# Kernel optimization log

Hardware: AMD Instinct MI355X
Metric: run time of the kernel (lower is better)

The kernel has to match this reference:

```python
import jax, jax.numpy as jnp
import numpy as np

B, S, D, H = 4, 2048, 512, 8
DEPTH = D // H
BAND = 16  # log_thresholds [1,2,4,8,16] union == distance <= 16


def setup_inputs() -> dict:
    key = jax.random.key(0)
    ks = jax.random.split(key, 11)
    sc = 0.02
    return {
        "q": jax.random.normal(ks[0], (B, S, D), jnp.float32),
        "k": jax.random.normal(ks[1], (B, S, D), jnp.float32),
        "v": jax.random.normal(ks[2], (B, S, D), jnp.float32),
        "wq": jax.random.normal(ks[3], (D, D), jnp.float32) * sc,
        "bq": jnp.zeros((D,), jnp.float32),
        "wk": jax.random.normal(ks[4], (D, D), jnp.float32) * sc,
        "bk": jnp.zeros((D,), jnp.float32),
        "wv": jax.random.normal(ks[5], (D, D), jnp.float32) * sc,
        "bv": jnp.zeros((D,), jnp.float32),
        "wo": jax.random.normal(ks[6], (D, D), jnp.float32) * sc,
        "bo": jnp.zeros((D,), jnp.float32),
    }


def _split_heads(x):
    # [B,S,D] -> [B,H,S,depth]
    b, s, _ = x.shape
    return x.reshape(b, s, H, DEPTH).transpose(0, 2, 1, 3)


def reference(q, k, v, wq, bq, wk, bk, wv, bv, wo, bo):
    qh = _split_heads(q @ wq + bq)
    kh = _split_heads(k @ wk + bk)
    vh = _split_heads(v @ wv + bv)
    scale = 1.0 / jnp.sqrt(jnp.float32(DEPTH))
    logits = jnp.einsum("bhqd,bhkd->bhqk", qh, kh) * scale  # [B,H,S,S]
    idx = jnp.arange(S)
    keep = jnp.abs(idx[:, None] - idx[None, :]) <= BAND  # band mask [S,S]
    logits = jnp.where(keep[None, None], logits, jnp.float32(-1e9))
    attn = jax.nn.softmax(logits, axis=-1)
    out = jnp.einsum("bhqk,bhkd->bhqd", attn, vh)
    out = out.transpose(0, 2, 1, 3).reshape(q.shape[0], -1, D)
    return out @ wo + bo
```

## Files before the change

### kernel.cpp

```cpp
#include <hip/hip_runtime.h>

typedef unsigned int uint;
typedef unsigned short ushort;
typedef __attribute__((ext_vector_type(8))) short bf16x8;
typedef __attribute__((ext_vector_type(4))) float f32x4;

namespace {
constexpr int kS = 2048;
constexpr int kD = 512;
constexpr int kH = 8;
constexpr int kBand = 16;

constexpr size_t kQpk = 0;
constexpr size_t kKpk = 4194304;
constexpr size_t kVpk = kKpk + 4259840;
constexpr size_t kObp = kVpk + 4259840;
constexpr size_t kApk = kObp + 4194304;
constexpr size_t kBpk = kApk + 12582912;
}

static __device__ __forceinline__ ushort f2bf(float f) {
  uint u = __builtin_bit_cast(uint, f);
  u = (u + 0x7fffu + ((u >> 16) & 1u)) >> 16;
  return (ushort)u;
}

static __device__ __forceinline__ bf16x8 cvt8(f32x4 lo, f32x4 hi) {
  uint4 r;
  asm("v_cvt_pk_bf16_f32 %0, %1, %2" : "=v"(r.x) : "v"(lo[0]), "v"(lo[1]));
  asm("v_cvt_pk_bf16_f32 %0, %1, %2" : "=v"(r.y) : "v"(lo[2]), "v"(lo[3]));
  asm("v_cvt_pk_bf16_f32 %0, %1, %2" : "=v"(r.z) : "v"(hi[0]), "v"(hi[1]));
  asm("v_cvt_pk_bf16_f32 %0, %1, %2" : "=v"(r.w) : "v"(hi[2]), "v"(hi[3]));
  return __builtin_bit_cast(bf16x8, r);
}

__global__ __launch_bounds__(256) void prep_all(
    const float* __restrict__ q, const float* __restrict__ k,
    const float* __restrict__ v, const float* __restrict__ wq,
    const float* __restrict__ wk, const float* __restrict__ wv,
    const float* __restrict__ wo, ushort* __restrict__ ws) {
  __shared__ float Ws[64][65];
  const int blk = blockIdx.x, tid = threadIdx.x;
  if (blk < 384) {
    const int z = blk >> 7, rb = blk & 127;
    const float* X = z == 0 ? q : (z == 1 ? k : v);
    ushort* A = ws + kApk + (size_t)z * 4194304 + (size_t)rb * 32768;
    const int tl = tid >> 2, dq = tid & 3;
    const float* src = X + (size_t)(rb * 64 + tl) * kD + dq * 8;
    ushort* dstb = A + (tl >> 4) * 512 + (dq * 16 + (tl & 15)) * 8;
#pragma unroll
    for (int c = 0; c < 16; ++c) {
      const f32x4 lo = *(const f32x4*)(src + c * 32);
      const f32x4 hi = *(const f32x4*)(src + c * 32 + 4);
      *(bf16x8*)(dstb + c * 2048) = cvt8(lo, hi);
    }
    return;
  }
  if (blk >= 640) {
    const int idx = blk - 640;
    const int bh = idx >> 1, gg = (idx & 1) * 64;
    ushort* p = ws + kVpk + ((size_t)(bh * 65 + gg) * 4) * 512 + tid * 8;
    *(uint4*)p = (uint4){0, 0, 0, 0};
    return;
  }
  const int w = blk - 384;
  const int z = w >> 6;
  const float* W = z == 0 ? wq : (z == 1 ? wk : (z == 2 ? wv : wo));
  const int kt = ((w >> 3) & 7) * 64, nt = (w & 7) * 64;
  const int r = tid >> 2, c0 = (tid & 3) * 16;
#pragma unroll
  for (int i = 0; i < 4; ++i) {
    const float4 x =
        *(const float4*)(W + (size_t)(kt + r) * kD + nt + c0 + i * 4);
    Ws[r][c0 + i * 4 + 0] = x.x;
    Ws[r][c0 + i * 4 + 1] = x.y;
    Ws[r][c0 + i * 4 + 2] = x.z;
    Ws[r][c0 + i * 4 + 3] = x.w;
  }
  __syncthreads();
  const int nl = tid >> 2, k0 = (tid & 3) * 16;
  alignas(16) ushort tmp[16];
#pragma unroll
  for (int i = 0; i < 16; ++i) tmp[i] = f2bf(Ws[k0 + i][nl]);
  const int ng = nt + nl, kg = kt + k0;
  const int c = ng >> 6, sub = (ng >> 4) & 3, l = ng & 15;
  const int it = kg >> 5, q0 = (kg >> 3) & 3;
  ushort* base = ws + kBpk + ((size_t)(z * 8 + c) * 16 + it) * 2048 +
                 (sub * 64 + l) * 8;
  *(uint4*)(base + q0 * 128) = *(const uint4*)&tmp[0];
  *(uint4*)(base + (q0 + 1) * 128) = *(const uint4*)&tmp[8];
}

__global__ __launch_bounds__(64) void gemm_qkv(
    const ushort* __restrict__ ws_c, ushort* __restrict__ ws,
    const float* __restrict__ bq, const float* __restrict__ bk,
    const float* __restrict__ bv) {
  __shared__ alignas(16) ushort Tl[64 * 72];

  const int lane = threadIdx.x, l15 = lane & 15, qd = lane >> 4;
  const int lin = blockIdx.x;
  const int xcd = lin & 7, j = lin >> 3;
  const int ct = j & 7;
  const int rtl = xcd + 8 * (j >> 3);
  const int mode = rtl >> 7, rt = rtl & 127;
  const int row0 = rt * 64;

  const float* bias = mode == 0 ? bq : (mode == 1 ? bk : bv);
  const ushort* pa =
      ws_c + kApk + (size_t)mode * 4194304 + (size_t)rt * 32768 + lane * 8;
  const ushort* pb =
      ws_c + kBpk + ((size_t)(mode * 8 + ct) * 16) * 2048 + lane * 8;

  f32x4 acc[4][4];
#pragma unroll
  for (int mi = 0; mi < 4; ++mi)
#pragma unroll
    for (int ni = 0; ni < 4; ++ni) acc[mi][ni] = (f32x4)(0.f);

  bf16x8 Af[3][4], Bf[3][4];
#define LDSET(s, itv)                                                  \
  {                                                                    \
    _Pragma("unroll") for (int x = 0; x < 4; ++x) {                    \
      Af[s][x] = *(const bf16x8*)(pa + (itv)*2048 + x * 512);          \
      Bf[s][x] = *(const bf16x8*)(pb + (itv)*2048 + x * 512);          \
    }                                                                  \
  }
  LDSET(0, 0);
  LDSET(1, 1);
#pragma unroll
  for (int it = 0; it < 16; ++it) {
    if (it < 14) LDSET((it + 2) % 3, it + 2);
    const int s = it % 3;
#pragma unroll
    for (int mi = 0; mi < 4; ++mi)
#pragma unroll
      for (int ni = 0; ni < 4; ++ni)
        acc[mi][ni] = __builtin_amdgcn_mfma_f32_16x16x32_bf16(
            Af[s][mi], Bf[s][ni], acc[mi][ni], 0, 0, 0);
  }
#undef LDSET

  float bcol[4];
#pragma unroll
  for (int ni = 0; ni < 4; ++ni) bcol[ni] = bias[ct * 64 + ni * 16 + l15];

  const int bh = (row0 >> 11) * kH + ct;
  if (mode <= 1) {
#pragma unroll
    for (int mi = 0; mi < 4; ++mi)
#pragma unroll
      for (int ni = 0; ni < 4; ++ni)
#pragma unroll
        for (int r = 0; r < 4; ++r)
          Tl[(mi * 16 + qd * 4 + r) * 72 + ni * 16 + l15] =
              f2bf(acc[mi][ni][r] + bcol[ni]);
    asm volatile("s_waitcnt lgkmcnt(0)" ::: "memory");
    const int s = (row0 & (kS - 1)) + lane;
    const int g = s >> 4;
    const ushort* Trow = &Tl[lane * 72];
    ushort* base =
        (mode == 0)
            ? ws + kQpk + ((size_t)(bh * 128 + g) * 2) * 512 + (s & 15) * 8
            : ws + kKpk + ((size_t)(bh * 130 + g + 1) * 2) * 512 + (s & 15) * 8;
#pragma unroll
    for (int cc = 0; cc < 8; ++cc)
      *(uint4*)(base + (cc >> 2) * 512 + (cc & 3) * 128) =
          *(const uint4*)&Trow[cc * 8];
  } else {
#pragma unroll
    for (int mi = 0; mi < 4; ++mi)
#pragma unroll
      for (int ni = 0; ni < 4; ++ni)
#pragma unroll
        for (int r = 0; r < 4; ++r)
          Tl[(ni * 16 + l15) * 72 + mi * 16 + qd * 4 + r] =
              f2bf(acc[mi][ni][r] + bcol[ni]);
    asm volatile("s_waitcnt lgkmcnt(0)" ::: "memory");
    const int nt = lane >> 4, l15v = lane & 15;
    const int sb = (row0 & (kS - 1)) + 16;
    const ushort* Trow = &Tl[lane * 72];
#pragma unroll
    for (int cc = 0; cc < 8; ++cc) {
      const int sc = sb + cc * 8;
      const int gg = sc >> 5, khc = (sc >> 3) & 3;
      ushort* dst = ws + kVpk + ((size_t)(bh * 65 + gg) * 4 + nt) * 512 +
                    khc * 128 + l15v * 8;
      *(uint4*)dst = *(const uint4*)&Trow[cc * 8];
    }
  }
}

__global__ __launch_bounds__(512) void attn_out(
    const ushort* __restrict__ ws_c, const float* __restrict__ bo,
    float* __restrict__ outp) {
  __shared__ alignas(16) ushort Pl[8 * 32 * 72];

  const int tid = threadIdx.x;
  const int w = tid >> 6, lane = tid & 63, l15 = lane & 15, qd = lane >> 4;
  const int b = blockIdx.y;
  const int q0 = blockIdx.x * 32;
  const int bh = b * kH + w;
  ushort* Plw = &Pl[w * 2304];

  const ushort* Qpk = ws_c + kQpk;
  const ushort* Kpk = ws_c + kKpk;
  const ushort* Vpk = ws_c + kVpk;

  bf16x8 qf[2][2], kf[4][2];
#pragma unroll
  for (int mi = 0; mi < 2; ++mi)
#pragma unroll
    for (int kc = 0; kc < 2; ++kc)
      qf[mi][kc] = *(const bf16x8*)&Qpk[((size_t)(bh * 128 + (q0 >> 4) + mi) *
                                            2 + kc) * 512 + lane * 8];
#pragma unroll
  for (int ni = 0; ni < 4; ++ni)
#pragma unroll
    for (int kc = 0; kc < 2; ++kc)
      kf[ni][kc] = *(const bf16x8*)&Kpk[((size_t)(bh * 130 + (q0 >> 4) + ni) *
                                            2 + kc) * 512 + lane * 8];

  f32x4 S[2][4];
#pragma unroll
  for (int mi = 0; mi < 2; ++mi)
#pragma unroll
    for (int ni = 0; ni < 4; ++ni) S[mi][ni] = (f32x4)(0.f);
#pragma unroll
  for (int mi = 0; mi < 2; ++mi)
#pragma unroll
    for (int ni = 0; ni < 4; ++ni)
#pragma unroll
      for (int kc = 0; kc < 2; ++kc)
        S[mi][ni] = __builtin_amdgcn_mfma_f32_16x16x32_bf16(
            qf[mi][kc], kf[ni][kc], S[mi][ni], 0, 0, 0);

#pragma unroll
  for (int mi = 0; mi < 2; ++mi)
#pragma unroll
    for (int ni = 0; ni < 4; ++ni)
#pragma unroll
      for (int r = 0; r < 4; ++r) {
        const int q_local = mi * 16 + qd * 4 + r;
        const int key_local = ni * 16 + l15;
        const int key = q0 - kBand + key_local;
        const int dlt = key_local - q_local;
        const bool ok = (dlt >= 0) && (dlt <= 32) && (key >= 0) && (key < kS);
        S[mi][ni][r] = ok ? S[mi][ni][r] * 0.125f : -3.0e38f;
      }

  float inv[2][4];
#pragma unroll
  for (int mi = 0; mi < 2; ++mi)
#pragma unroll
    for (int r = 0; r < 4; ++r) {
      float m = S[mi][0][r];
#pragma unroll
      for (int ni = 1; ni < 4; ++ni) m = fmaxf(m, S[mi][ni][r]);
      m = fmaxf(m, __shfl_xor(m, 1));
      m = fmaxf(m, __shfl_xor(m, 2));
      m = fmaxf(m, __shfl_xor(m, 4));
      m = fmaxf(m, __shfl_xor(m, 8));
      float s = 0.f;
#pragma unroll
      for (int ni = 0; ni < 4; ++ni) {
        const float e = __expf(S[mi][ni][r] - m);
        S[mi][ni][r] = e;
        s += e;
      }
      s += __shfl_xor(s, 1);
      s += __shfl_xor(s, 2);
      s += __shfl_xor(s, 4);
      s += __shfl_xor(s, 8);
      inv[mi][r] = 1.f / s;
    }

#pragma unroll
  for (int mi = 0; mi < 2; ++mi)
#pragma unroll
    for (int ni = 0; ni < 4; ++ni)
#pragma unroll
      for (int r = 0; r < 4; ++r)
        Plw[(mi * 16 + qd * 4 + r) * 72 + ni * 16 + l15] = f2bf(S[mi][ni][r]);
  asm volatile("s_waitcnt lgkmcnt(0)" ::: "memory");

  f32x4 O[2][4];
#pragma unroll
  for (int mi = 0; mi < 2; ++mi)
#pragma unroll
    for (int nt = 0; nt < 4; ++nt) O[mi][nt] = (f32x4)(0.f);

#pragma unroll
  for (int kc = 0; kc < 2; ++kc) {
    bf16x8 pf[2], vfr[4];
#pragma unroll
    for (int mi = 0; mi < 2; ++mi)
      pf[mi] = *(const bf16x8*)&Plw[(mi * 16 + l15) * 72 + kc * 32 + qd * 8];
#pragma unroll
    for (int nt = 0; nt < 4; ++nt)
      vfr[nt] = *(const bf16x8*)&Vpk[((size_t)(bh * 65 + (q0 >> 5) + kc) * 4 +
                                       nt) * 512 + lane * 8];
#pragma unroll
    for (int mi = 0; mi < 2; ++mi)
#pragma unroll
      for (int nt = 0; nt < 4; ++nt)
        O[mi][nt] = __builtin_amdgcn_mfma_f32_16x16x32_bf16(pf[mi], vfr[nt],
                                                            O[mi][nt], 0, 0, 0);
  }

#pragma unroll
  for (int mi = 0; mi < 2; ++mi)
#pragma unroll
    for (int nt = 0; nt < 4; ++nt)
#pragma unroll
      for (int r = 0; r < 4; ++r)
        Plw[(mi * 16 + qd * 4 + r) * 72 + nt * 16 + l15] =
            f2bf(O[mi][nt][r] * inv[mi][r]);

  __syncthreads();

  const ushort* pb =
      ws_c + kBpk + ((size_t)(3 * 8 + w) * 16) * 2048 + lane * 8;

  f32x4 acc[2][4];
#pragma unroll
  for (int mi = 0; mi < 2; ++mi)
#pragma unroll
    for (int ni = 0; ni < 4; ++ni) acc[mi][ni] = (f32x4)(0.f);

  bf16x8 Bf[2][4];
#pragma unroll
  for (int x = 0; x < 4; ++x) Bf[0][x] = *(const bf16x8*)(pb + x * 512);
#pragma unroll
  for (int it = 0; it < 16; ++it) {
    if (it < 15) {
#pragma unroll
      for (int x = 0; x < 4; ++x)
        Bf[(it + 1) & 1][x] =
            *(const bf16x8*)(pb + (size_t)(it + 1) * 2048 + x * 512);
    }
    bf16x8 af[2];
#pragma unroll
    for (int mi = 0; mi < 2; ++mi)
      af[mi] = *(const bf16x8*)&Pl[(it >> 1) * 2304 + (mi * 16 + l15) * 72 +
                                   (it & 1) * 32 + qd * 8];
#pragma unroll
    for (int mi = 0; mi < 2; ++mi)
#pragma unroll
      for (int ni = 0; ni < 4; ++ni)
        acc[mi][ni] = __builtin_amdgcn_mfma_f32_16x16x32_bf16(
            af[mi], Bf[it & 1][ni], acc[mi][ni], 0, 0, 0);
  }

#pragma unroll
  for (int ni = 0; ni < 4; ++ni) {
    const int colg = w * 64 + ni * 16 + l15;
    const float bc = bo[colg];
#pragma unroll
    for (int mi = 0; mi < 2; ++mi)
#pragma unroll
      for (int r = 0; r < 4; ++r) {
        const int token = b * kS + q0 + mi * 16 + qd * 4 + r;
        outp[(size_t)token * kD + colg] = acc[mi][ni][r] + bc;
      }
  }
}

extern "C" void kernel_launch(void* const* d_in, const int* in_sizes, int n_in,
                              void* d_out, int out_size, void* d_ws,
                              size_t ws_size, hipStream_t stream) {
  const float* q = (const float*)d_in[0];
  const float* k = (const float*)d_in[1];
  const float* v = (const float*)d_in[2];
  const float* wq = (const float*)d_in[3];
  const float* bq = (const float*)d_in[4];
  const float* wk = (const float*)d_in[5];
  const float* bk = (const float*)d_in[6];
  const float* wv = (const float*)d_in[7];
  const float* bv = (const float*)d_in[8];
  const float* wo = (const float*)d_in[9];
  const float* bo = (const float*)d_in[10];
  float* out = (float*)d_out;

  ushort* ws = (ushort*)d_ws;

  prep_all<<<dim3(704), 256, 0, stream>>>(q, k, v, wq, wk, wv, wo, ws);
  gemm_qkv<<<dim3(3072), 64, 0, stream>>>(ws, ws, bq, bk, bv);
  attn_out<<<dim3(kS / 32, 4), 512, 0, stream>>>(ws, bo, out);
}
```

Baseline: 149.1 us.

## Fuse fp32-to-bf16 activation conversion into QKV GEMM via LDS staging

```diff
diff --git a/kernel.cpp b/kernel.cpp
--- a/kernel.cpp
+++ b/kernel.cpp
@@ -3,6 +3,7 @@
 typedef unsigned int uint;
 typedef unsigned short ushort;
 typedef __attribute__((ext_vector_type(8))) short bf16x8;
+typedef __attribute__((ext_vector_type(4))) short bf16x4;
 typedef __attribute__((ext_vector_type(4))) float f32x4;
 
 namespace {
@@ -14,9 +15,7 @@
 constexpr size_t kQpk = 0;
 constexpr size_t kKpk = 4194304;
 constexpr size_t kVpk = kKpk + 4259840;
-constexpr size_t kObp = kVpk + 4259840;
-constexpr size_t kApk = kObp + 4194304;
-constexpr size_t kBpk = kApk + 12582912;
+constexpr size_t kBpk = kVpk + 4259840;
 }
 
 static __device__ __forceinline__ ushort f2bf(float f) {
@@ -34,36 +33,27 @@
   return __builtin_bit_cast(bf16x8, r);
 }
 
+static __device__ __forceinline__ bf16x4 cvt4(f32x4 x) {
+  uint2 r;
+  asm("v_cvt_pk_bf16_f32 %0, %1, %2" : "=v"(r.x) : "v"(x[0]), "v"(x[1]));
+  asm("v_cvt_pk_bf16_f32 %0, %1, %2" : "=v"(r.y) : "v"(x[2]), "v"(x[3]));
+  return __builtin_bit_cast(bf16x4, r);
+}
+
 __global__ __launch_bounds__(256) void prep_all(
-    const float* __restrict__ q, const float* __restrict__ k,
-    const float* __restrict__ v, const float* __restrict__ wq,
-    const float* __restrict__ wk, const float* __restrict__ wv,
-    const float* __restrict__ wo, ushort* __restrict__ ws) {
+    const float* __restrict__ wq, const float* __restrict__ wk,
+    const float* __restrict__ wv, const float* __restrict__ wo,
+    ushort* __restrict__ ws) {
   __shared__ float Ws[64][65];
   const int blk = blockIdx.x, tid = threadIdx.x;
-  if (blk < 384) {
-    const int z = blk >> 7, rb = blk & 127;
-    const float* X = z == 0 ? q : (z == 1 ? k : v);
-    ushort* A = ws + kApk + (size_t)z * 4194304 + (size_t)rb * 32768;
-    const int tl = tid >> 2, dq = tid & 3;
-    const float* src = X + (size_t)(rb * 64 + tl) * kD + dq * 8;
-    ushort* dstb = A + (tl >> 4) * 512 + (dq * 16 + (tl & 15)) * 8;
-#pragma unroll
-    for (int c = 0; c < 16; ++c) {
-      const f32x4 lo = *(const f32x4*)(src + c * 32);
-      const f32x4 hi = *(const f32x4*)(src + c * 32 + 4);
-      *(bf16x8*)(dstb + c * 2048) = cvt8(lo, hi);
-    }
-    return;
-  }
-  if (blk >= 640) {
-    const int idx = blk - 640;
+  if (blk >= 256) {
+    const int idx = blk - 256;
     const int bh = idx >> 1, gg = (idx & 1) * 64;
     ushort* p = ws + kVpk + ((size_t)(bh * 65 + gg) * 4) * 512 + tid * 8;
     *(uint4*)p = (uint4){0, 0, 0, 0};
     return;
   }
-  const int w = blk - 384;
+  const int w = blk;
   const int z = w >> 6;
   const float* W = z == 0 ? wq : (z == 1 ? wk : (z == 2 ? wv : wo));
   const int kt = ((w >> 3) & 7) * 64, nt = (w & 7) * 64;
@@ -92,10 +82,11 @@
 }
 
 __global__ __launch_bounds__(64) void gemm_qkv(
-    const ushort* __restrict__ ws_c, ushort* __restrict__ ws,
-    const float* __restrict__ bq, const float* __restrict__ bk,
-    const float* __restrict__ bv) {
-  __shared__ alignas(16) ushort Tl[64 * 72];
+    const float* __restrict__ q, const float* __restrict__ k,
+    const float* __restrict__ v, const ushort* __restrict__ ws_c,
+    ushort* __restrict__ ws, const float* __restrict__ bq,
+    const float* __restrict__ bk, const float* __restrict__ bv) {
+  __shared__ alignas(16) ushort smem[4608];
 
   const int lane = threadIdx.x, l15 = lane & 15, qd = lane >> 4;
   const int lin = blockIdx.x;
@@ -105,45 +96,81 @@
   const int mode = rtl >> 7, rt = rtl & 127;
   const int row0 = rt * 64;
 
+  const float* Ab = mode == 0 ? q : (mode == 1 ? k : v);
   const float* bias = mode == 0 ? bq : (mode == 1 ? bk : bv);
-  const ushort* pa =
-      ws_c + kApk + (size_t)mode * 4194304 + (size_t)rt * 32768 + lane * 8;
   const ushort* pb =
       ws_c + kBpk + ((size_t)(mode * 8 + ct) * 16) * 2048 + lane * 8;
 
+  const int g = lane >> 3, kc = lane & 7;
+  const float* pAld[8];
+#pragma unroll
+  for (int i = 0; i < 8; ++i)
+    pAld[i] = Ab + (size_t)(row0 + i * 8 + g) * kD + kc * 4;
+  const uint wbase = (uint)((kc >> 1) * 128 + g * 8 + (kc & 1) * 4);
+
   f32x4 acc[4][4];
 #pragma unroll
   for (int mi = 0; mi < 4; ++mi)
 #pragma unroll
     for (int ni = 0; ni < 4; ++ni) acc[mi][ni] = (f32x4)(0.f);
 
-  bf16x8 Af[3][4], Bf[3][4];
-#define LDSET(s, itv)                                                  \
-  {                                                                    \
-    _Pragma("unroll") for (int x = 0; x < 4; ++x) {                    \
-      Af[s][x] = *(const bf16x8*)(pa + (itv)*2048 + x * 512);          \
-      Bf[s][x] = *(const bf16x8*)(pb + (itv)*2048 + x * 512);          \
-    }                                                                  \
-  }
-  LDSET(0, 0);
-  LDSET(1, 1);
+  f32x4 Ld[8];
+  bf16x8 Bf[3][4];
+
+#pragma unroll
+  for (int i = 0; i < 8; ++i) Ld[i] = *(const f32x4*)(pAld[i]);
+#pragma unroll
+  for (int i = 0; i < 8; ++i)
+    *(bf16x4*)&smem[wbase + (i & 1) * 64 + (i >> 1) * 512] = cvt4(Ld[i]);
+#pragma unroll
+  for (int i = 0; i < 8; ++i) Ld[i] = *(const f32x4*)(pAld[i] + 32);
+#pragma unroll
+  for (int x = 0; x < 4; ++x) {
+    Bf[0][x] = *(const bf16x8*)(pb + x * 512);
+    Bf[1][x] = *(const bf16x8*)(pb + 2048 + x * 512);
+  }
+
 #pragma unroll
   for (int it = 0; it < 16; ++it) {
-    if (it < 14) LDSET((it + 2) % 3, it + 2);
+    asm volatile("s_waitcnt lgkmcnt(0)" ::: "memory");
+    __builtin_amdgcn_sched_barrier(0);
+    bf16x8 af[4];
+    const uint sb = (uint)(it & 1) * 2048;
+#pragma unroll
+    for (int mi = 0; mi < 4; ++mi)
+      af[mi] = *(const bf16x8*)&smem[sb + mi * 512 + (qd * 16 + l15) * 8];
+    if (it < 15) {
+      const uint sb1 = (uint)((it + 1) & 1) * 2048;
+#pragma unroll
+      for (int i = 0; i < 8; ++i)
+        *(bf16x4*)&smem[sb1 + wbase + (i & 1) * 64 + (i >> 1) * 512] =
+            cvt4(Ld[i]);
+    }
+    if (it < 14) {
+#pragma unroll
+      for (int i = 0; i < 8; ++i)
+        Ld[i] = *(const f32x4*)(pAld[i] + (it + 2) * 32);
+#pragma unroll
+      for (int x = 0; x < 4; ++x)
+        Bf[(it + 2) % 3][x] =
+            *(const bf16x8*)(pb + (size_t)(it + 2) * 2048 + x * 512);
+    }
     const int s = it % 3;
 #pragma unroll
     for (int mi = 0; mi < 4; ++mi)
 #pragma unroll
       for (int ni = 0; ni < 4; ++ni)
         acc[mi][ni] = __builtin_amdgcn_mfma_f32_16x16x32_bf16(
-            Af[s][mi], Bf[s][ni], acc[mi][ni], 0, 0, 0);
-  }
-#undef LDSET
+            af[mi], Bf[s][ni], acc[mi][ni], 0, 0, 0);
+  }
+  asm volatile("s_waitcnt lgkmcnt(0)" ::: "memory");
+  __builtin_amdgcn_sched_barrier(0);
 
   float bcol[4];
 #pragma unroll
   for (int ni = 0; ni < 4; ++ni) bcol[ni] = bias[ct * 64 + ni * 16 + l15];
 
+  ushort* Tl = smem;
   const int bh = (row0 >> 11) * kH + ct;
   if (mode <= 1) {
 #pragma unroll
@@ -156,12 +183,13 @@
               f2bf(acc[mi][ni][r] + bcol[ni]);
     asm volatile("s_waitcnt lgkmcnt(0)" ::: "memory");
     const int s = (row0 & (kS - 1)) + lane;
-    const int g = s >> 4;
+    const int gq = s >> 4;
     const ushort* Trow = &Tl[lane * 72];
     ushort* base =
         (mode == 0)
-            ? ws + kQpk + ((size_t)(bh * 128 + g) * 2) * 512 + (s & 15) * 8
-            : ws + kKpk + ((size_t)(bh * 130 + g + 1) * 2) * 512 + (s & 15) * 8;
+            ? ws + kQpk + ((size_t)(bh * 128 + gq) * 2) * 512 + (s & 15) * 8
+            : ws + kKpk + ((size_t)(bh * 130 + gq + 1) * 2) * 512 +
+                  (s & 15) * 8;
 #pragma unroll
     for (int cc = 0; cc < 8; ++cc)
       *(uint4*)(base + (cc >> 2) * 512 + (cc & 3) * 128) =
@@ -177,11 +205,11 @@
               f2bf(acc[mi][ni][r] + bcol[ni]);
     asm volatile("s_waitcnt lgkmcnt(0)" ::: "memory");
     const int nt = lane >> 4, l15v = lane & 15;
-    const int sb = (row0 & (kS - 1)) + 16;
+    const int sb2 = (row0 & (kS - 1)) + 16;
     const ushort* Trow = &Tl[lane * 72];
 #pragma unroll
     for (int cc = 0; cc < 8; ++cc) {
-      const int sc = sb + cc * 8;
+      const int sc = sb2 + cc * 8;
       const int gg = sc >> 5, khc = (sc >> 3) & 3;
       ushort* dst = ws + kVpk + ((size_t)(bh * 65 + gg) * 4 + nt) * 512 +
                     khc * 128 + l15v * 8;
@@ -383,7 +411,7 @@
 
   ushort* ws = (ushort*)d_ws;
 
-  prep_all<<<dim3(704), 256, 0, stream>>>(q, k, v, wq, wk, wv, wo, ws);
-  gemm_qkv<<<dim3(3072), 64, 0, stream>>>(ws, ws, bq, bk, bv);
+  prep_all<<<dim3(320), 256, 0, stream>>>(wq, wk, wv, wo, ws);
+  gemm_qkv<<<dim3(3072), 64, 0, stream>>>(q, k, v, ws, ws, bq, bk, bv);
   attn_out<<<dim3(kS / 32, 4), 512, 0, stream>>>(ws, bo, out);
 }
```

Measured after the change: 152.0 us. Within noise of the previous version (+2.0%).
